# Performance work log

Hardware: AMD Instinct MI355X
Metric: run time of the kernel (lower is better)

## Reference

```python
import jax, jax.numpy as jnp
import numpy as np


def setup_inputs() -> dict:
    key = jax.random.key(0)
    # [N, n, m]: batch, transform length (axis 1), columns
    x = jax.random.normal(key, (32, 1024, 512), dtype=jnp.float32)
    return {"x": x}


def reference(x):
    # Faithful port of idct_odd_case: IDCT-III via a length-2n complex IFFT
    # on a Hermitian-symmetric-style mirrored array, exactly as the TF code.
    N, n, m = x.shape
    k = jnp.arange(n, dtype=jnp.float32)
    # t[k] = sqrt(2n) * exp(i*pi*k/(2n)); t[0] scaled by extra sqrt(2)
    t = jnp.sqrt(2.0 * n) * jnp.exp(1j * k * (np.pi / (2.0 * n)))
    t = t.at[0].multiply(jnp.sqrt(2.0))
    W = t.astype(jnp.complex64)[None, :, None]           # [1, n, 1]
    xc = x.astype(jnp.complex64)
    yy_up = W * xc                                        # [N, n, m]
    # -i * W[1:n] * reverse(x[1:n]) along the transform axis
    yy_down = (-1j) * W[:, 1:, :] * xc[:, n - 1:0:-1, :]  # [N, n-1, m]
    yy_mid = jnp.zeros((N, 1, m), dtype=jnp.complex64)
    yy = jnp.concatenate([yy_up, yy_mid, yy_down], axis=1)  # [N, 2n, m]
    y = jnp.fft.ifft(yy, axis=1)                          # matlab_ifft: ifft on axis 1
    return jnp.real(y[:, :n, :]).astype(jnp.float32)
```

## Files before the change

### kernel.cpp

```cpp
#include <hip/hip_runtime.h>

typedef unsigned short u16;
typedef __attribute__((ext_vector_type(8))) __bf16 bf16x8;
typedef __attribute__((ext_vector_type(4))) float f32x4;

#define GLOAD_LDS16(g, l)                                                                     \
  __builtin_amdgcn_global_load_lds((const __attribute__((address_space(1))) unsigned int*)(g), \
                                   (__attribute__((address_space(3))) unsigned int*)(l), 16, 0, 0)

static __device__ __forceinline__ u16 f2bf(float f) {
  unsigned int u = __float_as_uint(f);
  u += 0x7fffu + ((u >> 16) & 1u);
  return (u16)(u >> 16);
}

#define BATCH 32
#define NN 1024
#define MM 512
#define KH 512

static __device__ __forceinline__ int swz(int r) { return ((r >> 1) ^ ((r & 1) << 2)) & 7; }

__global__ void fill_g(u16* __restrict__ G) {
  int idx = blockIdx.x * 256 + threadIdx.x;
  int j = idx >> 10;
  int r = idx & 1023;
  int s = r >> 6;
  int cp = (r >> 3) & 7;
  int sub = r & 7;
  int chunk = cp ^ swz(j);
  int k;
  if (chunk < 4) k = 2 * (s * 32 + chunk * 8 + sub);
  else           k = 2 * (s * 32 + (chunk - 4) * 8 + sub) + 1;
  float v;
  if (k == 0) {
    v = 0.03125f;
  } else {
    int ph = (k * (2 * j + 1)) & 4095;
    v = 0.04419417382415922f * cosf((float)ph * 1.5339807878856412e-3f);
  }
  G[idx] = f2bf(v);
}

__global__ __launch_bounds__(256, 2) void gemm_idct(const u16* __restrict__ G,
                                                    const float* __restrict__ X,
                                                    float* __restrict__ C) {
  __shared__ __align__(16) u16 sA[2][128 * 64];
  __shared__ __align__(16) u16 sX[128 * 64];
  const int wg   = blockIdx.x;
  const int xcd  = wg & 7;
  const int slot = wg >> 3;
  const int tm   = slot & 3;
  const int pair = ((slot >> 2) << 3) | xcd;
  const int tn   = pair & 3;
  const int b    = pair >> 2;

  const int t = threadIdx.x;
  const int wave = t >> 6, lane = t & 63;
  const int wr = wave >> 1, wc = wave & 1;
  const int lhi = lane >> 4, llo = lane & 15;

  const u16* srcA = G + ((size_t)(tm * 128 + (t >> 3)) << 10) + (t & 7) * 8;
#define ISSUE_A(s)                                                             \
  do {                                                                         \
    u16* dst = &sA[(s) & 1][0];                                                \
    _Pragma("unroll") for (int c = 0; c < 4; ++c)                              \
      GLOAD_LDS16(srcA + c * 32768 + (s) * 64, dst + c * 2048 + t * 8);        \
  } while (0)

  const int cp2 = (t & 63) << 1;
  const int kq  = t >> 6;
  const float* gX = X + ((size_t)b * NN + kq * 16) * MM + tn * 128 + cp2;

  float2 xr[16];
#define LOAD_X(s)                                                              \
  do {                                                                         \
    const float* p = gX + (size_t)(s) * 64 * MM;                               \
    _Pragma("unroll") for (int i = 0; i < 16; ++i)                             \
      xr[i] = *(const float2*)(p + (size_t)i * MM);                            \
  } while (0)

#define WRITE_X()                                                              \
  do {                                                                         \
    _Pragma("unroll") for (int cc = 0; cc < 2; ++cc) {                         \
      const int c = cp2 + cc;                                                  \
      const int fc = swz(c);                                                   \
      bf16x8 e, o;                                                             \
      _Pragma("unroll") for (int m = 0; m < 8; ++m) {                          \
        e[m] = (__bf16)(cc ? xr[2 * m].y : xr[2 * m].x);                       \
        o[m] = (__bf16)(cc ? xr[2 * m + 1].y : xr[2 * m + 1].x);               \
      }                                                                        \
      *(bf16x8*)&sX[c * 64 + ((kq ^ fc) << 3)] = e;                            \
      *(bf16x8*)&sX[c * 64 + (((4 + kq) ^ fc) << 3)] = o;                      \
    }                                                                          \
  } while (0)

  f32x4 accE[4][4] = {};
  f32x4 accO[4][4] = {};

  ISSUE_A(0);
  LOAD_X(0);
  __syncthreads();

  for (int s = 0; s < 16; ++s) {
    WRITE_X();
    __syncthreads();
    if (s < 15) {
      ISSUE_A(s + 1);
      LOAD_X(s + 1);
    }
    const u16* lA = &sA[s & 1][0];
    bf16x8 fe[4], fo[4], fxe[4], fxo[4];
#pragma unroll
    for (int i = 0; i < 4; ++i) {
      const int ra = wr * 64 + i * 16 + llo;
      const int rb = wc * 64 + i * 16 + llo;
      const int fa = swz(ra), fb = swz(rb);
      fe[i]  = *(const bf16x8*)&lA[ra * 64 + ((lhi ^ fa) << 3)];
      fo[i]  = *(const bf16x8*)&lA[ra * 64 + (((4 + lhi) ^ fa) << 3)];
      fxe[i] = *(const bf16x8*)&sX[rb * 64 + ((lhi ^ fb) << 3)];
      fxo[i] = *(const bf16x8*)&sX[rb * 64 + (((4 + lhi) ^ fb) << 3)];
    }
#pragma unroll
    for (int mi = 0; mi < 4; ++mi)
#pragma unroll
      for (int ni = 0; ni < 4; ++ni)
        accE[mi][ni] = __builtin_amdgcn_mfma_f32_16x16x32_bf16(
            fe[mi], fxe[ni], accE[mi][ni], 0, 0, 0);
#pragma unroll
    for (int mi = 0; mi < 4; ++mi)
#pragma unroll
      for (int ni = 0; ni < 4; ++ni)
        accO[mi][ni] = __builtin_amdgcn_mfma_f32_16x16x32_bf16(
            fo[mi], fxo[ni], accO[mi][ni], 0, 0, 0);
    __syncthreads();
  }

  float* Cb = C + (size_t)b * NN * MM;
  const int jhbase = tm * 128 + wr * 64 + lhi * 4;
  const int cbase  = tn * 128 + wc * 64 + llo;
#pragma unroll
  for (int mi = 0; mi < 4; ++mi)
#pragma unroll
    for (int ni = 0; ni < 4; ++ni) {
      const int jh = jhbase + mi * 16;
      const int c  = cbase + ni * 16;
#pragma unroll
      for (int r = 0; r < 4; ++r) {
        const float ye = accE[mi][ni][r];
        const float yo = accO[mi][ni][r];
        Cb[(size_t)(jh + r) * MM + c]            = ye + yo;
        Cb[(size_t)(NN - 1 - (jh + r)) * MM + c] = ye - yo;
      }
    }
#undef ISSUE_A
#undef LOAD_X
#undef WRITE_X
}

extern "C" void kernel_launch(void* const* d_in, const int* in_sizes, int n_in,
                              void* d_out, int out_size, void* d_ws, size_t ws_size,
                              hipStream_t stream) {
  const float* x = (const float*)d_in[0];
  float* out = (float*)d_out;
  u16* G = (u16*)d_ws;

  fill_g<<<dim3((512 * 1024) / 256), dim3(256), 0, stream>>>(G);
  gemm_idct<<<dim3(512), dim3(256), 0, stream>>>(G, x, out);
}
```

Measured before the change: 46.07 us.

## Retile IDCT GEMM into single-wave 64x32 blocks with register double-buffering

The GEMM moves from 256-thread workgroups computing 128x128 tiles to single-wave workgroups computing 64x32 tiles, launched as 4096 blocks instead of 512. Because each block is one wave, all __syncthreads barriers are replaced with explicit s_waitcnt and sched_barrier. X loads are double-buffered in registers so the next stage's global loads overlap the current MFMAs. G is relaid so each 64-row j-tile is contiguous per stage, which makes the LDS-direct copies linear. The goal is more waves per CU and less barrier stall, at the cost of more redundant X and G reads per output through L2.

```diff
diff --git a/kernel.cpp b/kernel.cpp
--- a/kernel.cpp
+++ b/kernel.cpp
@@ -23,15 +23,16 @@
 
 __global__ void fill_g(u16* __restrict__ G) {
   int idx = blockIdx.x * 256 + threadIdx.x;
-  int j = idx >> 10;
-  int r = idx & 1023;
-  int s = r >> 6;
-  int cp = (r >> 3) & 7;
-  int sub = r & 7;
-  int chunk = cp ^ swz(j);
+  int jt  = idx >> 16;
+  int s   = (idx >> 12) & 15;
+  int jl  = (idx >> 6) & 63;
+  int r64 = idx & 63;
+  int cp = r64 >> 3, sub = r64 & 7;
+  int dc = cp ^ swz(jl);
+  int j = jt * 64 + jl;
   int k;
-  if (chunk < 4) k = 2 * (s * 32 + chunk * 8 + sub);
-  else           k = 2 * (s * 32 + (chunk - 4) * 8 + sub) + 1;
+  if (dc < 4) k = 2 * (s * 32 + dc * 8 + sub);
+  else        k = 2 * (s * 32 + (dc - 4) * 8 + sub) + 1;
   float v;
   if (k == 0) {
     v = 0.03125f;
@@ -42,108 +43,110 @@
   G[idx] = f2bf(v);
 }
 
-__global__ __launch_bounds__(256, 2) void gemm_idct(const u16* __restrict__ G,
-                                                    const float* __restrict__ X,
-                                                    float* __restrict__ C) {
-  __shared__ __align__(16) u16 sA[2][128 * 64];
-  __shared__ __align__(16) u16 sX[128 * 64];
-  const int wg   = blockIdx.x;
-  const int xcd  = wg & 7;
-  const int slot = wg >> 3;
-  const int tm   = slot & 3;
-  const int pair = ((slot >> 2) << 3) | xcd;
-  const int tn   = pair & 3;
-  const int b    = pair >> 2;
+__global__ __launch_bounds__(64, 2) void gemm_idct(const u16* __restrict__ G,
+                                                   const float* __restrict__ X,
+                                                   float* __restrict__ C) {
+  __shared__ __align__(16) u16 sA[2][64 * 64];
+  __shared__ __align__(16) u16 sX[32 * 64];
+  const int wg    = blockIdx.x;
+  const int xcd   = wg & 7;
+  const int local = wg >> 3;
+  const int jt    = local & 7;
+  const int panel = xcd * 64 + (local >> 3);
+  const int ct    = panel & 15;
+  const int b     = panel >> 4;
 
-  const int t = threadIdx.x;
-  const int wave = t >> 6, lane = t & 63;
-  const int wr = wave >> 1, wc = wave & 1;
-  const int lhi = lane >> 4, llo = lane & 15;
+  const int l   = threadIdx.x;
+  const int llo = l & 15, lhi = l >> 4;
 
-  const u16* srcA = G + ((size_t)(tm * 128 + (t >> 3)) << 10) + (t & 7) * 8;
-#define ISSUE_A(s)                                                             \
-  do {                                                                         \
-    u16* dst = &sA[(s) & 1][0];                                                \
-    _Pragma("unroll") for (int c = 0; c < 4; ++c)                              \
-      GLOAD_LDS16(srcA + c * 32768 + (s) * 64, dst + c * 2048 + t * 8);        \
+  const u16* gA = G + (size_t)jt * 65536 + l * 8;
+#define ISSUE_A(s)                                                            \
+  do {                                                                        \
+    u16* dst = &sA[(s) & 1][0];                                               \
+    _Pragma("unroll") for (int cl = 0; cl < 8; ++cl)                          \
+      GLOAD_LDS16(gA + (s) * 4096 + cl * 512, dst + cl * 512 + l * 8);        \
   } while (0)
 
-  const int cp2 = (t & 63) << 1;
-  const int kq  = t >> 6;
-  const float* gX = X + ((size_t)b * NN + kq * 16) * MM + tn * 128 + cp2;
+  const float* gX = X + ((size_t)b * NN + lhi * 16) * MM + ct * 32 + 2 * llo;
 
-  float2 xr[16];
-#define LOAD_X(s)                                                              \
-  do {                                                                         \
-    const float* p = gX + (size_t)(s) * 64 * MM;                               \
-    _Pragma("unroll") for (int i = 0; i < 16; ++i)                             \
-      xr[i] = *(const float2*)(p + (size_t)i * MM);                            \
+#define LOAD_X(s, XR)                                                         \
+  do {                                                                        \
+    const float* p = gX + (size_t)(s) * 64 * MM;                              \
+    _Pragma("unroll") for (int i = 0; i < 16; ++i)                            \
+      XR[i] = *(const float2*)(p + (size_t)i * MM);                           \
   } while (0)
 
-#define WRITE_X()                                                              \
-  do {                                                                         \
-    _Pragma("unroll") for (int cc = 0; cc < 2; ++cc) {                         \
-      const int c = cp2 + cc;                                                  \
-      const int fc = swz(c);                                                   \
-      bf16x8 e, o;                                                             \
-      _Pragma("unroll") for (int m = 0; m < 8; ++m) {                          \
-        e[m] = (__bf16)(cc ? xr[2 * m].y : xr[2 * m].x);                       \
-        o[m] = (__bf16)(cc ? xr[2 * m + 1].y : xr[2 * m + 1].x);               \
-      }                                                                        \
-      *(bf16x8*)&sX[c * 64 + ((kq ^ fc) << 3)] = e;                            \
-      *(bf16x8*)&sX[c * 64 + (((4 + kq) ^ fc) << 3)] = o;                      \
-    }                                                                          \
+#define WRITE_X(XR)                                                           \
+  do {                                                                        \
+    _Pragma("unroll") for (int cc = 0; cc < 2; ++cc) {                        \
+      const int row = 2 * llo + cc;                                           \
+      const int f = swz(row);                                                 \
+      bf16x8 e, o;                                                            \
+      _Pragma("unroll") for (int m = 0; m < 8; ++m) {                         \
+        e[m] = (__bf16)(cc ? XR[2 * m].y : XR[2 * m].x);                      \
+        o[m] = (__bf16)(cc ? XR[2 * m + 1].y : XR[2 * m + 1].x);              \
+      }                                                                       \
+      *(bf16x8*)&sX[row * 64 + ((lhi ^ f) << 3)] = e;                         \
+      *(bf16x8*)&sX[row * 64 + (((4 + lhi) ^ f) << 3)] = o;                   \
+    }                                                                         \
   } while (0)
 
-  f32x4 accE[4][4] = {};
-  f32x4 accO[4][4] = {};
+  f32x4 accE[4][2] = {};
+  f32x4 accO[4][2] = {};
+  float2 xrA[16], xrB[16];
+
+#define STEP(s, XRC, XRN)                                                     \
+  do {                                                                        \
+    asm volatile("s_waitcnt vmcnt(0) lgkmcnt(0)" ::: "memory");               \
+    __builtin_amdgcn_sched_barrier(0);                                        \
+    WRITE_X(XRC);                                                             \
+    if ((s) < 15) {                                                           \
+      ISSUE_A((s) + 1);                                                       \
+      LOAD_X((s) + 1, XRN);                                                   \
+    }                                                                         \
+    asm volatile("s_waitcnt lgkmcnt(0)" ::: "memory");                        \
+    __builtin_amdgcn_sched_barrier(0);                                        \
+    const u16* lA = &sA[(s) & 1][0];                                          \
+    bf16x8 fe[4], fo[4], fxe[2], fxo[2];                                      \
+    _Pragma("unroll") for (int mi = 0; mi < 4; ++mi) {                        \
+      const int ra = mi * 16 + llo;                                           \
+      const int fa = swz(ra);                                                 \
+      fe[mi] = *(const bf16x8*)&lA[ra * 64 + ((lhi ^ fa) << 3)];              \
+      fo[mi] = *(const bf16x8*)&lA[ra * 64 + (((4 + lhi) ^ fa) << 3)];        \
+    }                                                                         \
+    _Pragma("unroll") for (int ni = 0; ni < 2; ++ni) {                        \
+      const int rb = ni * 16 + llo;                                           \
+      const int fb = swz(rb);                                                 \
+      fxe[ni] = *(const bf16x8*)&sX[rb * 64 + ((lhi ^ fb) << 3)];             \
+      fxo[ni] = *(const bf16x8*)&sX[rb * 64 + (((4 + lhi) ^ fb) << 3)];       \
+    }                                                                         \
+    _Pragma("unroll") for (int mi = 0; mi < 4; ++mi)                          \
+      _Pragma("unroll") for (int ni = 0; ni < 2; ++ni)                        \
+        accE[mi][ni] = __builtin_amdgcn_mfma_f32_16x16x32_bf16(               \
+            fe[mi], fxe[ni], accE[mi][ni], 0, 0, 0);                          \
+    _Pragma("unroll") for (int mi = 0; mi < 4; ++mi)                          \
+      _Pragma("unroll") for (int ni = 0; ni < 2; ++ni)                        \
+        accO[mi][ni] = __builtin_amdgcn_mfma_f32_16x16x32_bf16(               \
+            fo[mi], fxo[ni], accO[mi][ni], 0, 0, 0);                          \
+  } while (0)
 
   ISSUE_A(0);
-  LOAD_X(0);
-  __syncthreads();
+  LOAD_X(0, xrA);
 
-  for (int s = 0; s < 16; ++s) {
-    WRITE_X();
-    __syncthreads();
-    if (s < 15) {
-      ISSUE_A(s + 1);
-      LOAD_X(s + 1);
-    }
-    const u16* lA = &sA[s & 1][0];
-    bf16x8 fe[4], fo[4], fxe[4], fxo[4];
 #pragma unroll
-    for (int i = 0; i < 4; ++i) {
-      const int ra = wr * 64 + i * 16 + llo;
-      const int rb = wc * 64 + i * 16 + llo;
-      const int fa = swz(ra), fb = swz(rb);
-      fe[i]  = *(const bf16x8*)&lA[ra * 64 + ((lhi ^ fa) << 3)];
-      fo[i]  = *(const bf16x8*)&lA[ra * 64 + (((4 + lhi) ^ fa) << 3)];
-      fxe[i] = *(const bf16x8*)&sX[rb * 64 + ((lhi ^ fb) << 3)];
-      fxo[i] = *(const bf16x8*)&sX[rb * 64 + (((4 + lhi) ^ fb) << 3)];
-    }
-#pragma unroll
-    for (int mi = 0; mi < 4; ++mi)
-#pragma unroll
-      for (int ni = 0; ni < 4; ++ni)
-        accE[mi][ni] = __builtin_amdgcn_mfma_f32_16x16x32_bf16(
-            fe[mi], fxe[ni], accE[mi][ni], 0, 0, 0);
-#pragma unroll
-    for (int mi = 0; mi < 4; ++mi)
-#pragma unroll
-      for (int ni = 0; ni < 4; ++ni)
-        accO[mi][ni] = __builtin_amdgcn_mfma_f32_16x16x32_bf16(
-            fo[mi], fxo[ni], accO[mi][ni], 0, 0, 0);
-    __syncthreads();
+  for (int ss = 0; ss < 8; ++ss) {
+    STEP(2 * ss,     xrA, xrB);
+    STEP(2 * ss + 1, xrB, xrA);
   }
 
   float* Cb = C + (size_t)b * NN * MM;
-  const int jhbase = tm * 128 + wr * 64 + lhi * 4;
-  const int cbase  = tn * 128 + wc * 64 + llo;
+  const int jbase = jt * 64 + lhi * 4;
+  const int cbase = ct * 32 + llo;
 #pragma unroll
   for (int mi = 0; mi < 4; ++mi)
 #pragma unroll
-    for (int ni = 0; ni < 4; ++ni) {
-      const int jh = jhbase + mi * 16;
+    for (int ni = 0; ni < 2; ++ni) {
+      const int jh = jbase + mi * 16;
       const int c  = cbase + ni * 16;
 #pragma unroll
       for (int r = 0; r < 4; ++r) {
@@ -156,6 +159,7 @@
 #undef ISSUE_A
 #undef LOAD_X
 #undef WRITE_X
+#undef STEP
 }
 
 extern "C" void kernel_launch(void* const* d_in, const int* in_sizes, int n_in,
@@ -165,6 +169,6 @@
   float* out = (float*)d_out;
   u16* G = (u16*)d_ws;
 
-  fill_g<<<dim3((512 * 1024) / 256), dim3(256), 0, stream>>>(G);
-  gemm_idct<<<dim3(512), dim3(256), 0, stream>>>(G, x, out);
+  fill_g<<<dim3(524288 / 256), dim3(256), 0, stream>>>(G);
+  gemm_idct<<<dim3(4096), dim3(64), 0, stream>>>(G, x, out);
 }
```

New measurement: 62.20 us. +35.0%, slower.

## Halve N-tile, pre-tile G layout, double-buffer X registers with manual waitcnt

Applied to the files above, without the earlier changes.

The G matrix is stored pre-tiled per (row tile, k-step) so each k-step's A tile is one contiguous block. The column tile shrinks from 128 to 64, which doubles the grid to 1024 workgroups and changes the XCD mapping. X loads now run two steps ahead through two alternating register sets, with explicit s_waitcnt, raw barriers and setprio around the MFMA block for finer overlap. The cost is more G traffic per output and fragile hand-tuned wait counts.

```diff
diff --git a/kernel.cpp b/kernel.cpp
--- a/kernel.cpp
+++ b/kernel.cpp
@@ -17,21 +17,21 @@
 #define BATCH 32
 #define NN 1024
 #define MM 512
-#define KH 512
 
 static __device__ __forceinline__ int swz(int r) { return ((r >> 1) ^ ((r & 1) << 2)) & 7; }
 
 __global__ void fill_g(u16* __restrict__ G) {
   int idx = blockIdx.x * 256 + threadIdx.x;
-  int j = idx >> 10;
-  int r = idx & 1023;
-  int s = r >> 6;
-  int cp = (r >> 3) & 7;
-  int sub = r & 7;
-  int chunk = cp ^ swz(j);
+  int jt  = idx >> 17;
+  int s   = (idx >> 13) & 15;
+  int row = (idx >> 6) & 127;
+  int pc  = (idx >> 3) & 7;
+  int sub = idx & 7;
+  int dc = pc ^ (row & 7);
+  int j = jt * 128 + row;
   int k;
-  if (chunk < 4) k = 2 * (s * 32 + chunk * 8 + sub);
-  else           k = 2 * (s * 32 + (chunk - 4) * 8 + sub) + 1;
+  if (dc < 4) k = 2 * (s * 32 + dc * 8 + sub);
+  else        k = 2 * (s * 32 + (dc - 4) * 8 + sub) + 1;
   float v;
   if (k == 0) {
     v = 0.03125f;
@@ -45,117 +45,133 @@
 __global__ __launch_bounds__(256, 2) void gemm_idct(const u16* __restrict__ G,
                                                     const float* __restrict__ X,
                                                     float* __restrict__ C) {
-  __shared__ __align__(16) u16 sA[2][128 * 64];
-  __shared__ __align__(16) u16 sX[128 * 64];
-  const int wg   = blockIdx.x;
-  const int xcd  = wg & 7;
-  const int slot = wg >> 3;
-  const int tm   = slot & 3;
-  const int pair = ((slot >> 2) << 3) | xcd;
-  const int tn   = pair & 3;
-  const int b    = pair >> 2;
+  __shared__ __align__(16) u16 sA[2][8192];
+  __shared__ __align__(16) u16 sX[4096];
+  const int wg    = blockIdx.x;
+  const int xcd   = wg & 7;
+  const int local = wg >> 3;
+  const int jt    = local & 3;
+  const int pg    = xcd * 32 + (local >> 2);
+  const int ct    = pg & 7;
+  const int b     = pg >> 3;
 
   const int t = threadIdx.x;
   const int wave = t >> 6, lane = t & 63;
-  const int wr = wave >> 1, wc = wave & 1;
+  const int wm = wave >> 1, wn = wave & 1;
   const int lhi = lane >> 4, llo = lane & 15;
 
-  const u16* srcA = G + ((size_t)(tm * 128 + (t >> 3)) << 10) + (t & 7) * 8;
-#define ISSUE_A(s)                                                             \
+  const u16* gA = G + (size_t)jt * 131072 + t * 8;
+#define ISSUE_A(buf, s)                                                        \
   do {                                                                         \
-    u16* dst = &sA[(s) & 1][0];                                                \
-    _Pragma("unroll") for (int c = 0; c < 4; ++c)                              \
-      GLOAD_LDS16(srcA + c * 32768 + (s) * 64, dst + c * 2048 + t * 8);        \
+    _Pragma("unroll") for (int cl = 0; cl < 4; ++cl)                           \
+      GLOAD_LDS16(gA + (s) * 8192 + cl * 2048, &sA[buf][cl * 2048 + t * 8]);   \
   } while (0)
 
-  const int cp2 = (t & 63) << 1;
-  const int kq  = t >> 6;
-  const float* gX = X + ((size_t)b * NN + kq * 16) * MM + tn * 128 + cp2;
+  const int c2 = (t & 31) << 1;
+  const int kq = t >> 5;
+  const float* gX = X + ((size_t)b * NN + kq * 8) * MM + ct * 64 + c2;
 
-  float2 xr[16];
-#define LOAD_X(s)                                                              \
+#define LOAD_X(s, XR)                                                          \
   do {                                                                         \
     const float* p = gX + (size_t)(s) * 64 * MM;                               \
-    _Pragma("unroll") for (int i = 0; i < 16; ++i)                             \
-      xr[i] = *(const float2*)(p + (size_t)i * MM);                            \
+    _Pragma("unroll") for (int i = 0; i < 8; ++i)                              \
+      XR[i] = *(const float2*)(p + (size_t)i * MM);                            \
   } while (0)
 
-#define WRITE_X()                                                              \
+#define WRITE_X(XR)                                                            \
   do {                                                                         \
     _Pragma("unroll") for (int cc = 0; cc < 2; ++cc) {                         \
-      const int c = cp2 + cc;                                                  \
-      const int fc = swz(c);                                                   \
-      bf16x8 e, o;                                                             \
-      _Pragma("unroll") for (int m = 0; m < 8; ++m) {                          \
-        e[m] = (__bf16)(cc ? xr[2 * m].y : xr[2 * m].x);                       \
-        o[m] = (__bf16)(cc ? xr[2 * m + 1].y : xr[2 * m + 1].x);               \
-      }                                                                        \
-      *(bf16x8*)&sX[c * 64 + ((kq ^ fc) << 3)] = e;                            \
-      *(bf16x8*)&sX[c * 64 + (((4 + kq) ^ fc) << 3)] = o;                      \
+      const int row = c2 + cc;                                                 \
+      const int f = swz(row);                                                  \
+      ushort4 e, o;                                                            \
+      e.x = f2bf(cc ? XR[0].y : XR[0].x); o.x = f2bf(cc ? XR[1].y : XR[1].x);  \
+      e.y = f2bf(cc ? XR[2].y : XR[2].x); o.y = f2bf(cc ? XR[3].y : XR[3].x);  \
+      e.z = f2bf(cc ? XR[4].y : XR[4].x); o.z = f2bf(cc ? XR[5].y : XR[5].x);  \
+      e.w = f2bf(cc ? XR[6].y : XR[6].x); o.w = f2bf(cc ? XR[7].y : XR[7].x);  \
+      const int slot = (kq & 1) << 2;                                          \
+      *(ushort4*)&sX[row * 64 + (((kq >> 1) ^ f) << 3) + slot] = e;            \
+      *(ushort4*)&sX[row * 64 + (((4 + (kq >> 1)) ^ f) << 3) + slot] = o;      \
     }                                                                          \
   } while (0)
 
-  f32x4 accE[4][4] = {};
-  f32x4 accO[4][4] = {};
+  f32x4 accE[4][2] = {};
+  f32x4 accO[4][2] = {};
+  float2 xrA[8], xrB[8];
 
-  ISSUE_A(0);
-  LOAD_X(0);
-  __syncthreads();
+#define STEP(s, XR)                                                            \
+  do {                                                                         \
+    WRITE_X(XR);          \
+    if ((s) < 15)                                                              \
+      asm volatile("s_waitcnt vmcnt(8) lgkmcnt(0)" ::: "memory");              \
+    else                                                                       \
+      asm volatile("s_waitcnt vmcnt(0) lgkmcnt(0)" ::: "memory");              \
+    __builtin_amdgcn_sched_barrier(0);                                         \
+    __builtin_amdgcn_s_barrier();         \
+    __builtin_amdgcn_sched_barrier(0);                                         \
+    if ((s) < 15) ISSUE_A(((s) + 1) & 1, (s) + 1);                             \
+    if ((s) < 14) LOAD_X((s) + 2, XR);                                         \
+    {                                                                          \
+      const u16* lA = &sA[(s) & 1][0];                                         \
+      bf16x8 fe[4], fo[4], fxe[2], fxo[2];                                     \
+      _Pragma("unroll") for (int mf = 0; mf < 4; ++mf) {                       \
+        const int ra = wm * 64 + mf * 16 + llo;                                \
+        const int fa = ra & 7;                                                 \
+        fe[mf] = *(const bf16x8*)&lA[ra * 64 + ((lhi ^ fa) << 3)];             \
+        fo[mf] = *(const bf16x8*)&lA[ra * 64 + (((4 + lhi) ^ fa) << 3)];       \
+      }                                                                        \
+      _Pragma("unroll") for (int nf = 0; nf < 2; ++nf) {                       \
+        const int rb = wn * 32 + nf * 16 + llo;                                \
+        const int fb = swz(rb);                                                \
+        fxe[nf] = *(const bf16x8*)&sX[rb * 64 + ((lhi ^ fb) << 3)];            \
+        fxo[nf] = *(const bf16x8*)&sX[rb * 64 + (((4 + lhi) ^ fb) << 3)];      \
+      }                                                                        \
+      __builtin_amdgcn_s_setprio(1);                                           \
+      _Pragma("unroll") for (int mf = 0; mf < 4; ++mf)                         \
+        _Pragma("unroll") for (int nf = 0; nf < 2; ++nf)                       \
+          accE[mf][nf] = __builtin_amdgcn_mfma_f32_16x16x32_bf16(              \
+              fe[mf], fxe[nf], accE[mf][nf], 0, 0, 0);                         \
+      _Pragma("unroll") for (int mf = 0; mf < 4; ++mf)                         \
+        _Pragma("unroll") for (int nf = 0; nf < 2; ++nf)                       \
+          accO[mf][nf] = __builtin_amdgcn_mfma_f32_16x16x32_bf16(              \
+              fo[mf], fxo[nf], accO[mf][nf], 0, 0, 0);                         \
+      __builtin_amdgcn_s_setprio(0);                                           \
+    }                                                                          \
+    __builtin_amdgcn_sched_barrier(0);                                         \
+    __builtin_amdgcn_s_barrier();                                \
+    __builtin_amdgcn_sched_barrier(0);                                         \
+  } while (0)
 
-  for (int s = 0; s < 16; ++s) {
-    WRITE_X();
-    __syncthreads();
-    if (s < 15) {
-      ISSUE_A(s + 1);
-      LOAD_X(s + 1);
-    }
-    const u16* lA = &sA[s & 1][0];
-    bf16x8 fe[4], fo[4], fxe[4], fxo[4];
+  LOAD_X(0, xrA);
+  ISSUE_A(0, 0);
+  LOAD_X(1, xrB);
+
 #pragma unroll
-    for (int i = 0; i < 4; ++i) {
-      const int ra = wr * 64 + i * 16 + llo;
-      const int rb = wc * 64 + i * 16 + llo;
-      const int fa = swz(ra), fb = swz(rb);
-      fe[i]  = *(const bf16x8*)&lA[ra * 64 + ((lhi ^ fa) << 3)];
-      fo[i]  = *(const bf16x8*)&lA[ra * 64 + (((4 + lhi) ^ fa) << 3)];
-      fxe[i] = *(const bf16x8*)&sX[rb * 64 + ((lhi ^ fb) << 3)];
-      fxo[i] = *(const bf16x8*)&sX[rb * 64 + (((4 + lhi) ^ fb) << 3)];
-    }
-#pragma unroll
-    for (int mi = 0; mi < 4; ++mi)
-#pragma unroll
-      for (int ni = 0; ni < 4; ++ni)
-        accE[mi][ni] = __builtin_amdgcn_mfma_f32_16x16x32_bf16(
-            fe[mi], fxe[ni], accE[mi][ni], 0, 0, 0);
-#pragma unroll
-    for (int mi = 0; mi < 4; ++mi)
-#pragma unroll
-      for (int ni = 0; ni < 4; ++ni)
-        accO[mi][ni] = __builtin_amdgcn_mfma_f32_16x16x32_bf16(
-            fo[mi], fxo[ni], accO[mi][ni], 0, 0, 0);
-    __syncthreads();
+  for (int ss = 0; ss < 8; ++ss) {
+    STEP(2 * ss,     xrA);
+    STEP(2 * ss + 1, xrB);
   }
 
   float* Cb = C + (size_t)b * NN * MM;
-  const int jhbase = tm * 128 + wr * 64 + lhi * 4;
-  const int cbase  = tn * 128 + wc * 64 + llo;
+  const int cbase = ct * 64 + wn * 32 + llo;
 #pragma unroll
-  for (int mi = 0; mi < 4; ++mi)
+  for (int mf = 0; mf < 4; ++mf)
 #pragma unroll
-    for (int ni = 0; ni < 4; ++ni) {
-      const int jh = jhbase + mi * 16;
-      const int c  = cbase + ni * 16;
+    for (int nf = 0; nf < 2; ++nf) {
+      const int jh0 = jt * 128 + wm * 64 + mf * 16 + lhi * 4;
+      const int c   = cbase + nf * 16;
 #pragma unroll
       for (int r = 0; r < 4; ++r) {
-        const float ye = accE[mi][ni][r];
-        const float yo = accO[mi][ni][r];
-        Cb[(size_t)(jh + r) * MM + c]            = ye + yo;
-        Cb[(size_t)(NN - 1 - (jh + r)) * MM + c] = ye - yo;
+        const float ye = accE[mf][nf][r];
+        const float yo = accO[mf][nf][r];
+        const int j = jh0 + r;
+        Cb[(size_t)j * MM + c]            = ye + yo;
+        Cb[(size_t)(NN - 1 - j) * MM + c] = ye - yo;
       }
     }
 #undef ISSUE_A
 #undef LOAD_X
 #undef WRITE_X
+#undef STEP
 }
 
 extern "C" void kernel_launch(void* const* d_in, const int* in_sizes, int n_in,
@@ -165,6 +181,6 @@
   float* out = (float*)d_out;
   u16* G = (u16*)d_ws;
 
-  fill_g<<<dim3((512 * 1024) / 256), dim3(256), 0, stream>>>(G);
-  gemm_idct<<<dim3(512), dim3(256), 0, stream>>>(G, x, out);
+  fill_g<<<dim3(2048), dim3(256), 0, stream>>>(G);
+  gemm_idct<<<dim3(1024), dim3(256), 0, stream>>>(G, x, out);
 }
```

Result: slower. 49.04 us (+6.4%).
